# Performance work log

Hardware: AMD Instinct MI355X
Metric: run time of the kernel (lower is better)

## Reference

```python
import jax, jax.numpy as jnp
import numpy as np

FACTOR = 5

def setup_inputs() -> dict:
    key = jax.random.key(0)
    k1, k2, k3 = jax.random.split(key, 3)
    B, L, H, D = 4, 2048, 8, 64
    logL = int(np.ceil(np.log(L)))          # 8
    U_part = min(2 * FACTOR * logL, L)      # 80 sampled keys per query
    queries = jax.random.normal(k1, (B, L, H, D), dtype=jnp.float32)
    keys = jax.random.normal(k2, (B, L, H, D), dtype=jnp.float32)
    index_sample = jax.random.randint(k3, (L, U_part), 0, L)
    return {"queries": queries, "keys": keys, "index_sample": index_sample}

def reference(queries, keys, index_sample):
    B, L, H, D = queries.shape
    q = jnp.transpose(queries, (0, 2, 1, 3))   # [B,H,L,D]
    k = jnp.transpose(keys, (0, 2, 1, 3))      # [B,H,L,D]
    logL = int(np.ceil(np.log(L)))
    u = min(FACTOR * logL, L)                  # n_top queries

    # sample keys per query position: [B,H,L,S,D]
    K_sample = k[:, :, index_sample, :]
    # Q_i . K_sample_ij : [B,H,L,S]
    QK_sample = jnp.einsum('bhld,bhlsd->bhls', q, K_sample)
    # sparsity measure M = max - mean (mean over full L as in source)
    M = QK_sample.max(axis=-1) - QK_sample.sum(axis=-1) / L   # [B,H,L]
    _, M_top = jax.lax.top_k(M, u)                            # [B,H,u]

    # gather selected queries and compute full scores against all keys
    Q_reduce = jnp.take_along_axis(q, M_top[..., None], axis=2)  # [B,H,u,D]
    scale = 1.0 / jnp.sqrt(jnp.float32(D))
    scores = jnp.einsum('bhud,bhld->bhul', Q_reduce, k) * scale  # [B,H,u,L]
    attn = jax.nn.softmax(scores, axis=-1)

    # scatter softmaxed rows into full [B,H,L,L] attention matrix (rest zeros)
    out = jnp.zeros((B, H, L, L), dtype=attn.dtype)
    b_idx = jnp.arange(B)[:, None, None]
    h_idx = jnp.arange(H)[None, :, None]
    out = out.at[b_idx, h_idx, M_top, :].set(attn)
    return out
```

## Files before the change

kernel.cpp:

```cpp
#include <hip/hip_runtime.h>
#include <math.h>

#define NB 4
#define NL 2048
#define NH 8
#define ND 64
#define NUPART 80
#define NUTOP 40
#define NROWS (NB * NH * NL)
#define NATTN (NB * NH * NUTOP)
#define Z1ROWS 12288
#define NZ3 (NROWS - Z1ROWS)
#define K3BLK (NZ3 / 4)
#define Z1F4 (Z1ROWS * 512)
#define G1 (16384 * 256)
#define Z3F4 (NZ3 * 512)
#define G3 (K3BLK * 256)

typedef float vfloat4 __attribute__((ext_vector_type(4)));

__global__ __launch_bounds__(256) void k_compute_M_zero(
    const float* __restrict__ q, const float* __restrict__ k,
    const int* __restrict__ idx, float* __restrict__ M,
    float* __restrict__ out)
{
    const int t = threadIdx.x;

    {
        const int g = blockIdx.x * 256 + t;
        vfloat4* o = (vfloat4*)out;
        const vfloat4 z = (vfloat4)(0.0f);
        o[g] = z;
        const int g2 = g + G1;
        if (g2 < Z1F4) o[g2] = z;
    }

    const int w    = blockIdx.x * 4 + (t >> 6);
    const int lane = t & 63;
    const int l    = w & (NL - 1);
    const int bh   = w >> 11;
    const int h    = bh & (NH - 1);
    const int b    = bh >> 3;
    const int sl   = lane >> 2;
    const int dg   = lane & 3;
    const int d0   = dg * 16;

    const float4* qv = (const float4*)(q + (((size_t)(b * NL + l) * NH + h) * ND + d0));
    const float4 q0 = qv[0], q1 = qv[1], q2 = qv[2], q3 = qv[3];

    float mx = -INFINITY, sm = 0.0f;
#pragma unroll
    for (int r = 0; r < 5; ++r) {
        const int s  = r * 16 + sl;
        const int ki = idx[l * NUPART + s];
        const float4* kv = (const float4*)(k + (((size_t)(b * NL + ki) * NH + h) * ND + d0));
        const float4 k0 = kv[0], k1 = kv[1], k2 = kv[2], k3 = kv[3];
        float p = q0.x * k0.x + q0.y * k0.y + q0.z * k0.z + q0.w * k0.w
                + q1.x * k1.x + q1.y * k1.y + q1.z * k1.z + q1.w * k1.w
                + q2.x * k2.x + q2.y * k2.y + q2.z * k2.z + q2.w * k2.w
                + q3.x * k3.x + q3.y * k3.y + q3.z * k3.z + q3.w * k3.w;
        p += __shfl_xor(p, 1);
        p += __shfl_xor(p, 2);
        mx = fmaxf(mx, p);
        sm += p;
    }
#pragma unroll
    for (int m = 4; m < 64; m <<= 1) {
        mx = fmaxf(mx, __shfl_xor(mx, m));
        sm += __shfl_xor(sm, m);
    }
    if (lane == 0) M[w] = mx - sm * (1.0f / (float)NL);
}

__global__ __launch_bounds__(256) void k_topk(
    const float* __restrict__ M, int* __restrict__ rowmap,
    int* __restrict__ Mtop)
{
    __shared__ float sM[NL];
    __shared__ float rv[4];
    __shared__ int   ri[4];
    const int bh = blockIdx.x;
    const int t  = threadIdx.x;

    for (int j = t; j < NL; j += 256) {
        sM[j] = M[bh * NL + j];
        rowmap[bh * NL + j] = 0;
    }
    __syncthreads();

    for (int it = 0; it < NUTOP; ++it) {
        float v = -INFINITY;
        int   i = NL;
        for (int j = t; j < NL; j += 256) {
            const float m = sM[j];
            if (m > v || (m == v && j < i)) { v = m; i = j; }
        }
#pragma unroll
        for (int off = 1; off < 64; off <<= 1) {
            const float ov = __shfl_xor(v, off);
            const int   oi = __shfl_xor(i, off);
            if (ov > v || (ov == v && oi < i)) { v = ov; i = oi; }
        }
        const int wid = t >> 6;
        if ((t & 63) == 0) { rv[wid] = v; ri[wid] = i; }
        __syncthreads();
        if (t == 0) {
            for (int w2 = 1; w2 < 4; ++w2) {
                if (rv[w2] > v || (rv[w2] == v && ri[w2] < i)) { v = rv[w2]; i = ri[w2]; }
            }
            Mtop[bh * NUTOP + it] = i;
            rowmap[bh * NL + i] = 1;
            sM[i] = -INFINITY;
        }
        __syncthreads();
    }
}

__global__ __launch_bounds__(256) void k_scores(
    const float* __restrict__ q, const float* __restrict__ k,
    const int* __restrict__ Mtop, float* __restrict__ scores)
{
    __shared__ float4 qs[NUTOP][16];
    __shared__ int    rows[NUTOP];

    const int bh = blockIdx.x >> 3;
    const int ct = blockIdx.x & 7;
    const int b  = bh >> 3;
    const int h  = bh & 7;
    const int t  = threadIdx.x;

    if (t < NUTOP) rows[t] = Mtop[bh * NUTOP + t];
    __syncthreads();
    for (int i = t; i < NUTOP * 16; i += 256) {
        const int r = i >> 4, d = i & 15;
        qs[r][d] = ((const float4*)q)[((size_t)(b * NL + rows[r]) * NH + h) * 16 + d];
    }
    __syncthreads();

    const int c = ct * 256 + t;
    const float4* kv = (const float4*)k + ((size_t)(b * NL + c) * NH + h) * 16;
    float4 kc[16];
#pragma unroll
    for (int i = 0; i < 16; ++i) kc[i] = kv[i];

    float* srow = scores + (size_t)bh * NUTOP * NL + c;
    for (int r = 0; r < NUTOP; ++r) {
        float s = 0.0f;
#pragma unroll
        for (int i = 0; i < 16; ++i) {
            const float4 qq = qs[r][i];
            s += qq.x * kc[i].x + qq.y * kc[i].y + qq.z * kc[i].z + qq.w * kc[i].w;
        }
        srow[(size_t)r * NL] = s * 0.125f;
    }
}

__global__ __launch_bounds__(256) void k_zero_attn(
    const int* __restrict__ rowmap, const int* __restrict__ Mtop,
    const float* __restrict__ scores, float* __restrict__ out)
{
    const int t = threadIdx.x;

    {
        const int g = blockIdx.x * 256 + t;
        vfloat4* base = (vfloat4*)out + (size_t)Z1ROWS * 512;
        const vfloat4 z = (vfloat4)(0.0f);
#pragma unroll
        for (int s = 0; s < 8; ++s) {
            const int p = g + s * G3;
            const int row = p >> 9;
            if (!rowmap[Z1ROWS + row]) base[p] = z;
        }
    }

    if (blockIdx.x % 10 == 2) {
        const int a = blockIdx.x / 10;
        if (a < NATTN) {
            __shared__ float redm[4];
            __shared__ float reds[4];
            const int bh   = a / NUTOP;
            const int ui   = a % NUTOP;
            const int row  = Mtop[bh * NUTOP + ui];
            const int lane = t & 63;
            const int wid  = t >> 6;

            const float* srow = scores + ((size_t)bh * NUTOP + ui) * NL;
            float sc[8];
            float mx = -INFINITY;
#pragma unroll
            for (int j = 0; j < 8; ++j) {
                sc[j] = srow[t + 256 * j];
                mx = fmaxf(mx, sc[j]);
            }
#pragma unroll
            for (int off = 1; off < 64; off <<= 1) mx = fmaxf(mx, __shfl_xor(mx, off));
            if (lane == 0) redm[wid] = mx;
            __syncthreads();
            mx = fmaxf(fmaxf(redm[0], redm[1]), fmaxf(redm[2], redm[3]));

            float lsum = 0.0f;
#pragma unroll
            for (int j = 0; j < 8; ++j) {
                sc[j] = __expf(sc[j] - mx);
                lsum += sc[j];
            }
#pragma unroll
            for (int off = 1; off < 64; off <<= 1) lsum += __shfl_xor(lsum, off);
            if (lane == 0) reds[wid] = lsum;
            __syncthreads();
            const float inv = 1.0f / (reds[0] + reds[1] + reds[2] + reds[3]);

            float* orow = out + ((size_t)bh * NL + row) * NL;
#pragma unroll
            for (int j = 0; j < 8; ++j) orow[t + 256 * j] = sc[j] * inv;
        }
    }
}

extern "C" void kernel_launch(void* const* d_in, const int* in_sizes, int n_in,
                              void* d_out, int out_size, void* d_ws, size_t ws_size,
                              hipStream_t stream) {
    const float* q   = (const float*)d_in[0];
    const float* k   = (const float*)d_in[1];
    const int*   idx = (const int*)d_in[2];
    float* out = (float*)d_out;

    float* Mws    = (float*)d_ws;
    int*   rowmap = (int*)((char*)d_ws + (256 << 10));
    int*   Mtop   = (int*)((char*)d_ws + (512 << 10));
    float* scores = (float*)((char*)d_ws + (1 << 20));

    k_compute_M_zero<<<NROWS / 4, 256, 0, stream>>>(q, k, idx, Mws, out);
    k_topk<<<NB * NH, 256, 0, stream>>>(Mws, rowmap, Mtop);
    k_scores<<<NB * NH * 8, 256, 0, stream>>>(q, k, Mtop, scores);
    k_zero_attn<<<K3BLK, 256, 0, stream>>>(rowmap, Mtop, scores, out);
}
```

Measured before the change: 340.1 us.

## Spread output zero-fill across top-k and scores kernels to fill idle GPU

The zero-fill of the large output matrix is split into four regions. Two new regions are handled by extra blocks added to the top-k kernel and the scores kernel, which otherwise launch only 32 and 256 blocks. The aim is to use the idle compute units during those small serial kernels for bandwidth-bound zero stores, which shrinks the zeroing work left for the first and last kernels. Region sizes are rebalanced so that all rows are still covered exactly once before the softmax rows are written.

```diff
diff --git a/kernel.cpp b/kernel.cpp
--- a/kernel.cpp
+++ b/kernel.cpp
@@ -9,13 +9,17 @@
 #define NUTOP 40
 #define NROWS (NB * NH * NL)
 #define NATTN (NB * NH * NUTOP)
-#define Z1ROWS 12288
-#define NZ3 (NROWS - Z1ROWS)
-#define K3BLK (NZ3 / 4)
-#define Z1F4 (Z1ROWS * 512)
-#define G1 (16384 * 256)
-#define Z3F4 (NZ3 * 512)
-#define G3 (K3BLK * 256)
+
+#define ZA_ROWS 10240
+#define ZB_ROWS 1536
+#define ZC_ROWS 1536
+#define ZD_BASE (ZA_ROWS + ZB_ROWS + ZC_ROWS)
+#define ZD_ROWS (NROWS - ZD_BASE)
+
+#define ZA_F4 (ZA_ROWS * 512)
+#define K1_THREADS (16384 * 256)
+#define K3B_BLOCKS 13056
+#define G3 (K3B_BLOCKS * 256)
 
 typedef float vfloat4 __attribute__((ext_vector_type(4)));
 
@@ -31,8 +35,8 @@
         vfloat4* o = (vfloat4*)out;
         const vfloat4 z = (vfloat4)(0.0f);
         o[g] = z;
-        const int g2 = g + G1;
-        if (g2 < Z1F4) o[g2] = z;
+        const int g2 = g + K1_THREADS;
+        if (g2 < ZA_F4) o[g2] = z;
     }
 
     const int w    = blockIdx.x * 4 + (t >> 6);
@@ -72,15 +76,23 @@
     if (lane == 0) M[w] = mx - sm * (1.0f / (float)NL);
 }
 
-__global__ __launch_bounds__(256) void k_topk(
+__global__ __launch_bounds__(256) void k_topk_zero(
     const float* __restrict__ M, int* __restrict__ rowmap,
-    int* __restrict__ Mtop)
-{
+    int* __restrict__ Mtop, float* __restrict__ out)
+{
+    const int t = threadIdx.x;
+
+    if (blockIdx.x >= NB * NH) {
+        const int g = (blockIdx.x - NB * NH) * 256 + t;
+        vfloat4* o = (vfloat4*)out + (size_t)ZA_ROWS * 512 + g;
+        *o = (vfloat4)(0.0f);
+        return;
+    }
+
     __shared__ float sM[NL];
     __shared__ float rv[4];
     __shared__ int   ri[4];
     const int bh = blockIdx.x;
-    const int t  = threadIdx.x;
 
     for (int j = t; j < NL; j += 256) {
         sM[j] = M[bh * NL + j];
@@ -116,10 +128,20 @@
     }
 }
 
-__global__ __launch_bounds__(256) void k_scores(
+__global__ __launch_bounds__(256) void k_scores_zero(
     const float* __restrict__ q, const float* __restrict__ k,
-    const int* __restrict__ Mtop, float* __restrict__ scores)
-{
+    const int* __restrict__ Mtop, float* __restrict__ scores,
+    float* __restrict__ out)
+{
+    const int t = threadIdx.x;
+
+    if (blockIdx.x >= 256) {
+        const int g = (blockIdx.x - 256) * 256 + t;
+        vfloat4* o = (vfloat4*)out + ((size_t)ZA_ROWS + ZB_ROWS) * 512 + g;
+        *o = (vfloat4)(0.0f);
+        return;
+    }
+
     __shared__ float4 qs[NUTOP][16];
     __shared__ int    rows[NUTOP];
 
@@ -127,7 +149,6 @@
     const int ct = blockIdx.x & 7;
     const int b  = bh >> 3;
     const int h  = bh & 7;
-    const int t  = threadIdx.x;
 
     if (t < NUTOP) rows[t] = Mtop[bh * NUTOP + t];
     __syncthreads();
@@ -163,13 +184,13 @@
 
     {
         const int g = blockIdx.x * 256 + t;
-        vfloat4* base = (vfloat4*)out + (size_t)Z1ROWS * 512;
+        vfloat4* base = (vfloat4*)out + (size_t)ZD_BASE * 512;
         const vfloat4 z = (vfloat4)(0.0f);
 #pragma unroll
         for (int s = 0; s < 8; ++s) {
             const int p = g + s * G3;
             const int row = p >> 9;
-            if (!rowmap[Z1ROWS + row]) base[p] = z;
+            if (!rowmap[ZD_BASE + row]) base[p] = z;
         }
     }
 
@@ -231,7 +252,7 @@
     float* scores = (float*)((char*)d_ws + (1 << 20));
 
     k_compute_M_zero<<<NROWS / 4, 256, 0, stream>>>(q, k, idx, Mws, out);
-    k_topk<<<NB * NH, 256, 0, stream>>>(Mws, rowmap, Mtop);
-    k_scores<<<NB * NH * 8, 256, 0, stream>>>(q, k, Mtop, scores);
-    k_zero_attn<<<K3BLK, 256, 0, stream>>>(rowmap, Mtop, scores, out);
-}
+    k_topk_zero<<<NB * NH + 3072, 256, 0, stream>>>(Mws, rowmap, Mtop, out);
+    k_scores_zero<<<256 + 3072, 256, 0, stream>>>(q, k, Mtop, scores, out);
+    k_zero_attn<<<K3B_BLOCKS, 256, 0, stream>>>(rowmap, Mtop, scores, out);
+}
```

Result: no change. 340.0 us (-0.0%).
